# Kernel tuning notes

Measured on AMD Instinct MI355X. Metric: run time of the kernel, lower is better.

## Reference

```python
import jax, jax.numpy as jnp
import numpy as np

N = 80000
E = 1280000
C_IN, HID, C_OUT = 3, 64, 1
DEPTH = 3
KS = [40000, 20000, 10000]  # ceil(0.5 * n) per pooling level
EPS = 1e-5


def gcn_conv(x, W, src, dst, ew, n, fill=2.0):
    # PyG GCNConv with add_self_loops=True; improved => self-loop weight fill=2.0
    h = x @ W                                           # [n, F]
    deg = jax.ops.segment_sum(ew, dst, num_segments=n) + fill
    dinv = jax.lax.rsqrt(deg)
    norm = dinv[src] * ew * dinv[dst]                   # [E]
    agg = jax.ops.segment_sum(norm[:, None] * h[src], dst, num_segments=n)
    return agg + (fill * dinv * dinv)[:, None] * h      # self-loop term


def batchnorm(x, gamma, beta):
    # BatchNorm1d in training mode: biased batch stats over the node dim
    mu = jnp.mean(x, axis=0)
    var = jnp.var(x, axis=0)
    return gamma * (x - mu) * jax.lax.rsqrt(var + EPS) + beta


def gcn_block(x, src, dst, ew, n, W, gamma, beta, fill=2.0):
    return jax.nn.relu(batchnorm(gcn_conv(x, W, src, dst, ew, n, fill), gamma, beta))


def topk_pool(x, src, dst, ew, w, k):
    # TopKPooling with ReLU nonlinearity: score = relu(x.w / ||w||)
    n = x.shape[0]
    score = jax.nn.relu(x @ w / jnp.linalg.norm(w))
    sc, perm = jax.lax.top_k(score, k)
    xk = x[perm] * sc[:, None]
    # filter_adj with fixed edge count: invalid edges get weight 0 (no-op in GCN)
    mapping = jnp.full((n,), -1, dtype=src.dtype).at[perm].set(
        jnp.arange(k, dtype=src.dtype))
    ns, nd = mapping[src], mapping[dst]
    valid = (ns >= 0) & (nd >= 0)
    ns = jnp.where(valid, ns, 0)
    nd = jnp.where(valid, nd, 0)
    new_ew = jnp.where(valid, ew, jnp.zeros((), ew.dtype))
    return xk, ns, nd, new_ew, perm


def _forward(x, edge_index, Wd, gd, bd, pw, Wu, gu, bu, W_out):
    src, dst = edge_index[0], edge_index[1]
    ew = jnp.ones(src.shape, x.dtype)
    n = x.shape[0]
    x = gcn_block(x, src, dst, ew, n, Wd[0], gd[0], bd[0])
    xs, sds, ews, perms = [x], [(src, dst)], [ew], []
    for i in range(DEPTH):
        x, src, dst, ew, perm = topk_pool(x, src, dst, ew, pw[i], KS[i])
        x = gcn_block(x, src, dst, ew, KS[i], Wd[i + 1], gd[i + 1], bd[i + 1])
        if i < DEPTH - 1:
            xs.append(x); sds.append((src, dst)); ews.append(ew)
        perms.append(perm)
    for i in range(DEPTH):
        j = DEPTH - 1 - i
        res = xs[j]; src, dst = sds[j]; ew = ews[j]; perm = perms[j]
        up = jnp.zeros_like(res).at[perm].set(x)
        x = res + up
        if i < DEPTH - 1:
            x = gcn_block(x, src, dst, ew, res.shape[0], Wu[i], gu[i], bu[i])
        else:
            x = jax.nn.sigmoid(
                gcn_conv(x, W_out, src, dst, ew, res.shape[0], fill=1.0))
    return x


def setup_inputs() -> dict:
    key = jax.random.key(0)
    ks = jax.random.split(key, 16)
    nrm = lambda k, shape: jax.random.normal(k, shape, jnp.float32) * 0.1
    inp = {
        "x": jax.random.normal(ks[0], (N, C_IN), jnp.float32),
        "edge_index": jax.random.randint(ks[1], (2, E), 0, N, jnp.int32),
    }
    dims = [(C_IN, HID)] + [(HID, HID)] * DEPTH
    ki = 2
    for l, (a, b) in enumerate(dims):
        inp[f"W_d{l}"] = nrm(ks[ki], (a, b)); ki += 1
        inp[f"g_d{l}"] = jnp.ones((b,), jnp.float32)
        inp[f"b_d{l}"] = jnp.zeros((b,), jnp.float32)
    for l in range(DEPTH):
        inp[f"pw{l}"] = nrm(ks[ki], (HID,)); ki += 1
    for l in range(DEPTH - 1):
        inp[f"W_u{l}"] = nrm(ks[ki], (HID, HID)); ki += 1
        inp[f"g_u{l}"] = jnp.ones((HID,), jnp.float32)
        inp[f"b_u{l}"] = jnp.zeros((HID,), jnp.float32)
    inp["W_out"] = nrm(ks[ki], (HID, C_OUT))
    return inp


def reference(x, edge_index, W_d0, g_d0, b_d0, W_d1, g_d1, b_d1, W_d2, g_d2,
              b_d2, W_d3, g_d3, b_d3, pw0, pw1, pw2, W_u0, g_u0, b_u0,
              W_u1, g_u1, b_u1, W_out):
    Wd = [W_d0, W_d1, W_d2, W_d3]
    gd = [g_d0, g_d1, g_d2, g_d3]
    bd = [b_d0, b_d1, b_d2, b_d3]
    pw = [pw0, pw1, pw2]
    Wu = [W_u0, W_u1]
    gu = [g_u0, g_u1]
    bu = [b_u0, b_u1]
    return _forward(x, edge_index, Wd, gd, bd, pw, Wu, gu, bu, W_out)
```

## Files before the change

### kernel.cpp

```cpp
#include <hip/hip_runtime.h>
#include <cstdint>
#include <utility>

#define NN0 80000
#define NE 1280000
#define MMB_GRID 2048
#define EB 2048
#define ENB 625

static inline int cdiv(int a, int b){ return (a+b-1)/b; }

__global__ void k_conv64(const int* __restrict__ rp, const int* __restrict__ col,
                         const float* __restrict__ dinv, const float* __restrict__ x,
                         const float* __restrict__ W, float* __restrict__ out,
                         float* __restrict__ part, int n){
  __shared__ float yl[4][64];
  __shared__ float ls[64], lq[64];
  int lane = threadIdx.x & 63, w = threadIdx.x >> 6;
  if (threadIdx.x < 64){ ls[threadIdx.x] = 0.f; lq[threadIdx.x] = 0.f; }
  __syncthreads();
  float sa = 0.f, sq = 0.f;
  int wid = blockIdx.x*4 + w, nw = gridDim.x*4;
  for (int i = wid; i < n; i += nw){
    int beg = rp[i], end = rp[i+1];
    float di = dinv[i];
    float y = 0.f;
    int j = beg;
    for (; j + 4 <= end; j += 4){
      int s0 = col[j], s1 = col[j+1], s2 = col[j+2], s3 = col[j+3];
      float y0 = dinv[s0]*x[s0*64+lane];
      float y1 = dinv[s1]*x[s1*64+lane];
      float y2 = dinv[s2]*x[s2*64+lane];
      float y3 = dinv[s3]*x[s3*64+lane];
      y += (y0+y1) + (y2+y3);
    }
    for (; j < end; j++){ int s = col[j]; y += dinv[s]*x[s*64+lane]; }
    y = di*y + 2.f*di*di*x[i*64+lane];
    yl[w][lane] = y;
    float acc = 0.f;
    #pragma unroll
    for (int k2 = 0; k2 < 64; k2++)
      acc += yl[w][k2]*W[k2*64+lane];
    out[i*64+lane] = acc;
    sa += acc; sq += acc*acc;
  }
  atomicAdd(&ls[lane], sa); atomicAdd(&lq[lane], sq);
  __syncthreads();
  if (threadIdx.x < 128)
    part[blockIdx.x*128 + threadIdx.x] =
      (threadIdx.x < 64) ? ls[threadIdx.x] : lq[threadIdx.x-64];
}

__global__ void k_conv3(const int* __restrict__ rp, const int* __restrict__ col,
                        const float* __restrict__ dinv, const float* __restrict__ x,
                        const float* __restrict__ W, float* __restrict__ out,
                        float* __restrict__ part, int n){
  __shared__ float ls[64], lq[64];
  int lane = threadIdx.x & 63, w = threadIdx.x >> 6;
  if (threadIdx.x < 64){ ls[threadIdx.x] = 0.f; lq[threadIdx.x] = 0.f; }
  __syncthreads();
  float wf0 = W[lane], wf1 = W[64+lane], wf2 = W[128+lane];
  float sa = 0.f, sq = 0.f;
  int wid = blockIdx.x*4 + w, nw = gridDim.x*4;
  for (int i = wid; i < n; i += nw){
    int beg = rp[i], end = rp[i+1];
    float a0 = 0.f, a1 = 0.f, a2 = 0.f;
    for (int j = beg + lane; j < end; j += 64){
      int s2 = col[j];
      float ds = dinv[s2];
      a0 += ds*x[s2*3+0]; a1 += ds*x[s2*3+1]; a2 += ds*x[s2*3+2];
    }
    for (int o = 32; o > 0; o >>= 1){
      a0 += __shfl_xor(a0, o); a1 += __shfl_xor(a1, o); a2 += __shfl_xor(a2, o);
    }
    float di = dinv[i];
    float sl = 2.f*di*di;
    a0 = di*a0 + sl*x[i*3+0];
    a1 = di*a1 + sl*x[i*3+1];
    a2 = di*a2 + sl*x[i*3+2];
    float s = a0*wf0 + a1*wf1 + a2*wf2;
    out[i*64+lane] = s; sa += s; sq += s*s;
  }
  atomicAdd(&ls[lane], sa); atomicAdd(&lq[lane], sq);
  __syncthreads();
  if (threadIdx.x < 128)
    part[blockIdx.x*128 + threadIdx.x] =
      (threadIdx.x < 64) ? ls[threadIdx.x] : lq[threadIdx.x-64];
}

__global__ void k_stats_reduce(const float* __restrict__ part, float* __restrict__ stats){
  int c = blockIdx.x, lane = threadIdx.x;
  float s = 0.f;
  for (int b = lane; b < MMB_GRID; b += 64) s += part[b*128 + c];
  for (int o = 32; o > 0; o >>= 1) s += __shfl_xor(s, o);
  if (lane == 0) stats[c] = s;
}

__global__ void k_matvec(const float* __restrict__ x, const float* __restrict__ W,
                         float* __restrict__ h1, int n){
  int lane = threadIdx.x & 63, w = threadIdx.x >> 6;
  int wid = blockIdx.x*4 + w, nw = gridDim.x*4;
  float wv = W[lane];
  for (int i = wid; i < n; i += nw){
    float v = x[i*64+lane]*wv;
    for (int o = 32; o > 0; o >>= 1) v += __shfl_xor(v, o);
    if (lane == 0) h1[i] = v;
  }
}

__global__ void k_ehist6(const int* __restrict__ key, int* __restrict__ hist, int shift){
  __shared__ int lh[64];
  if (threadIdx.x < 64) lh[threadIdx.x] = 0;
  __syncthreads();
  int base = blockIdx.x*EB + threadIdx.x;
  #pragma unroll
  for (int u = 0; u < 8; u++)
    atomicAdd(&lh[(key[base + u*256] >> shift) & 63], 1);
  __syncthreads();
  if (threadIdx.x < 64) hist[threadIdx.x*ENB + blockIdx.x] = lh[threadIdx.x];
}

__global__ void k_escatter6(const int* __restrict__ keyin, const int* __restrict__ valin,
                            int* __restrict__ keyout, int* __restrict__ valout,
                            const int* __restrict__ hist, int shift){
  __shared__ int dbase[64], run[64], wcnt[4][64];
  int t = threadIdx.x, lane = t & 63, w = t >> 6;
  if (t < 64){ dbase[t] = hist[t*ENB + blockIdx.x]; run[t] = 0; }
  __syncthreads();
  for (int u = 0; u < 8; u++){
    if (t < 64){ wcnt[0][t]=0; wcnt[1][t]=0; wcnt[2][t]=0; wcnt[3][t]=0; }
    __syncthreads();
    int g = blockIdx.x*EB + u*256 + t;
    int kk = keyin[g], vv = valin[g];
    int d = (kk >> shift) & 63;
    unsigned long long m = ~0ull;
    #pragma unroll
    for (int b = 0; b < 6; b++){
      unsigned long long bal = __ballot((d >> b) & 1);
      m &= ((d >> b) & 1) ? bal : ~bal;
    }
    int rnk = __popcll(m & ((1ull << lane) - 1ull));
    if (rnk == 0) wcnt[w][d] = __popcll(m);
    __syncthreads();
    int off2 = run[d] + rnk;
    for (int w2 = 0; w2 < w; w2++) off2 += wcnt[w2][d];
    int pos = dbase[d] + off2;
    keyout[pos] = kk; valout[pos] = vv;
    __syncthreads();
    if (t < 64) run[t] += wcnt[0][t] + wcnt[1][t] + wcnt[2][t] + wcnt[3][t];
    __syncthreads();
  }
}

__global__ void k_rp_search(const int* __restrict__ skey, int* __restrict__ rp,
                            float* __restrict__ dinvA, float* __restrict__ dinvB, int n){
  int i = blockIdx.x*blockDim.x + threadIdx.x;
  if (i >= n) return;
  int lo = 0, hi = NE;
  while (lo < hi){ int mid = (lo+hi)>>1; if (skey[mid] < i) lo = mid+1; else hi = mid; }
  int a = lo;
  lo = a; hi = NE;
  while (lo < hi){ int mid = (lo+hi)>>1; if (skey[mid] < i+1) lo = mid+1; else hi = mid; }
  int b2 = lo;
  rp[i] = a;
  if (i == n-1) rp[n] = NE;
  float deg = (float)(b2 - a);
  dinvA[i] = 1.0f/sqrtf(deg + 2.f);
  dinvB[i] = 1.0f/sqrtf(deg + 1.f);
}

__global__ void k_scan_part(const int* __restrict__ in, int* __restrict__ bsum, int n){
  __shared__ int ws[256];
  int base = blockIdx.x*2048 + threadIdx.x*8;
  int s = 0;
  #pragma unroll
  for (int u = 0; u < 8; u++){ int i = base+u; if (i < n) s += in[i]; }
  ws[threadIdx.x] = s; __syncthreads();
  for (int st = 128; st > 0; st >>= 1){
    if (threadIdx.x < st) ws[threadIdx.x] += ws[threadIdx.x+st];
    __syncthreads();
  }
  if (threadIdx.x == 0) bsum[blockIdx.x] = ws[0];
}

__global__ void k_scan_fin_rp(const int* __restrict__ in, const int* __restrict__ bsum, int nb,
                              int* __restrict__ rp, float* __restrict__ dinvA, int n){
  __shared__ int bws[256]; __shared__ int ws[256];
  int t = threadIdx.x;
  bws[t] = (t < nb) ? bsum[t] : 0; __syncthreads();
  for (int st = 1; st < 256; st <<= 1){
    int a = (t >= st) ? bws[t-st] : 0; __syncthreads();
    bws[t] += a; __syncthreads();
  }
  int blockoff = (blockIdx.x == 0) ? 0 : bws[blockIdx.x-1];
  int base = blockIdx.x*2048 + t*8;
  int v[8]; int s = 0;
  #pragma unroll
  for (int u = 0; u < 8; u++){ int i = base+u; v[u] = (i < n) ? in[i] : 0; s += v[u]; }
  ws[t] = s; __syncthreads();
  for (int st = 1; st < 256; st <<= 1){
    int a = (t >= st) ? ws[t-st] : 0; __syncthreads();
    ws[t] += a; __syncthreads();
  }
  int off = blockoff + ws[t] - s;
  #pragma unroll
  for (int u = 0; u < 8; u++){
    int i = base+u;
    if (i < n){
      rp[i] = off; off += v[u];
      dinvA[i] = 1.0f/sqrtf((float)v[u] + 2.f);
      if (i == n-1) rp[n] = off;
    }
  }
}

__global__ void k_scan_fin_flat(int* __restrict__ data, const int* __restrict__ bsum, int nb, int n){
  __shared__ int bws[256]; __shared__ int ws[256];
  int t = threadIdx.x;
  bws[t] = (t < nb) ? bsum[t] : 0; __syncthreads();
  for (int st = 1; st < 256; st <<= 1){
    int a = (t >= st) ? bws[t-st] : 0; __syncthreads();
    bws[t] += a; __syncthreads();
  }
  int blockoff = (blockIdx.x == 0) ? 0 : bws[blockIdx.x-1];
  int base = blockIdx.x*2048 + t*8;
  int v[8]; int s = 0;
  #pragma unroll
  for (int u = 0; u < 8; u++){ int i = base+u; v[u] = (i < n) ? data[i] : 0; s += v[u]; }
  ws[t] = s; __syncthreads();
  for (int st = 1; st < 256; st <<= 1){
    int a = (t >= st) ? ws[t-st] : 0; __syncthreads();
    ws[t] += a; __syncthreads();
  }
  int off = blockoff + ws[t] - s;
  #pragma unroll
  for (int u = 0; u < 8; u++){
    int i = base+u;
    if (i < n){ data[i] = off; off += v[u]; }
  }
}

__global__ void k_hist_mapped(const int* __restrict__ rp_p, const int* __restrict__ col_p,
                              const int* __restrict__ mapv, int* __restrict__ indeg, int np){
  int d = blockIdx.x*blockDim.x + threadIdx.x;
  if (d >= np) return;
  int md = mapv[d];
  if (md < 0) return;
  int c = 0, e = rp_p[d+1];
  int j = rp_p[d];
  for (; j + 4 <= e; j += 4){
    int c0 = (mapv[col_p[j]]   >= 0);
    int c1 = (mapv[col_p[j+1]] >= 0);
    int c2 = (mapv[col_p[j+2]] >= 0);
    int c3 = (mapv[col_p[j+3]] >= 0);
    c += (c0+c1) + (c2+c3);
  }
  for (; j < e; j++) if (mapv[col_p[j]] >= 0) c++;
  indeg[md] = c;
}
__global__ void k_scatter_mapped(const int* __restrict__ rp_p, const int* __restrict__ col_p,
                                 const int* __restrict__ mapv, const int* __restrict__ rp_c,
                                 int* __restrict__ col_c, int np){
  int d = blockIdx.x*blockDim.x + threadIdx.x;
  if (d >= np) return;
  int md = mapv[d];
  if (md < 0) return;
  int pos = rp_c[md], e = rp_p[d+1];
  int j = rp_p[d];
  for (; j + 4 <= e; j += 4){
    int m0 = mapv[col_p[j]], m1 = mapv[col_p[j+1]];
    int m2 = mapv[col_p[j+2]], m3 = mapv[col_p[j+3]];
    if (m0 >= 0) col_c[pos++] = m0;
    if (m1 >= 0) col_c[pos++] = m1;
    if (m2 >= 0) col_c[pos++] = m2;
    if (m3 >= 0) col_c[pos++] = m3;
  }
  for (; j < e; j++){
    int ms = mapv[col_p[j]];
    if (ms >= 0) col_c[pos++] = ms;
  }
}

__global__ void k_gather_sig(const int* __restrict__ rp, const int* __restrict__ col,
                             const float* __restrict__ dinv, const float* __restrict__ h1,
                             float* __restrict__ out, int n){
  int i = blockIdx.x*blockDim.x + threadIdx.x;
  if (i >= n) return;
  int beg = rp[i], end = rp[i+1];
  float di = dinv[i];
  float acc = 0.f;
  int j = beg;
  for (; j + 4 <= end; j += 4){
    int s0 = col[j], s1 = col[j+1], s2 = col[j+2], s3 = col[j+3];
    float v0 = dinv[s0]*h1[s0];
    float v1 = dinv[s1]*h1[s1];
    float v2 = dinv[s2]*h1[s2];
    float v3 = dinv[s3]*h1[s3];
    acc += (v0+v1) + (v2+v3);
  }
  for (; j < end; j++) acc += dinv[col[j]]*h1[col[j]];
  float v = di*acc + di*di*h1[i];
  out[i] = 1.f/(1.f+expf(-v));
}

__global__ void k_bnrelu_scatter(const float* __restrict__ x, const float* __restrict__ stats,
                                 const float* __restrict__ gamma, const float* __restrict__ beta,
                                 const int* __restrict__ perm, float* __restrict__ res, int n){
  int t = blockIdx.x*blockDim.x + threadIdx.x;
  if (t >= n*64) return;
  int r = t >> 6, f = t & 63;
  float inv_n = 1.0f/(float)n;
  float mu = stats[f]*inv_n;
  float var = stats[64+f]*inv_n - mu*mu;
  float v = gamma[f]*(x[t]-mu)*(1.0f/sqrtf(var+1e-5f)) + beta[f];
  res[perm[r]*64+f] += fmaxf(v, 0.f);
}

__global__ void k_bnrelu_score(float* __restrict__ x, const float* __restrict__ stats,
                               const float* __restrict__ gamma, const float* __restrict__ beta,
                               const float* __restrict__ pw,
                               float* __restrict__ score, unsigned* __restrict__ key,
                               int* __restrict__ idx, int n, int P){
  int lane = threadIdx.x & 63, w = threadIdx.x >> 6;
  int wid = blockIdx.x*4 + w, nw = gridDim.x*4;
  float inv_n = 1.f/(float)n;
  float mu = stats[lane]*inv_n;
  float var = stats[64+lane]*inv_n - mu*mu;
  float gs = gamma[lane]*(1.f/sqrtf(var+1e-5f));
  float bt = beta[lane];
  float pv = pw[lane];
  float q = pv*pv;
  for (int o = 32; o > 0; o >>= 1) q += __shfl_xor(q, o);
  float qn = 1.f/sqrtf(q);
  for (int i = wid; i < n; i += nw){
    float v = fmaxf(gs*(x[i*64+lane]-mu)+bt, 0.f);
    x[i*64+lane] = v;
    float s = v*pv;
    for (int o = 32; o > 0; o >>= 1) s += __shfl_xor(s, o);
    if (lane == 0){
      float sc = fmaxf(s*qn, 0.f);
      score[i] = sc; key[i] = ~__float_as_uint(sc); idx[i] = i;
    }
  }
  for (int g = n + wid; g < P; g += nw)
    if (lane == 0){ key[g] = 0xFFFFFFFFu; idx[g] = 0; }
}

__global__ void k_radix_hist(const unsigned* __restrict__ key, int* __restrict__ hist,
                             int shift, int nblk){
  __shared__ int lh[256];
  lh[threadIdx.x] = 0; __syncthreads();
  int base = blockIdx.x*1024 + threadIdx.x;
  #pragma unroll
  for (int u = 0; u < 4; u++){
    unsigned d = (key[base + u*256] >> shift) & 255u;
    atomicAdd(&lh[d], 1);
  }
  __syncthreads();
  hist[threadIdx.x*nblk + blockIdx.x] = lh[threadIdx.x];
}

__global__ void k_radix_scatter(const unsigned* __restrict__ keyin, const int* __restrict__ idxin,
                                unsigned* __restrict__ keyout, int* __restrict__ idxout,
                                const int* __restrict__ hist, int shift, int nblk){
  __shared__ int dbase[256], run[256], sc[256];
  __shared__ int wcnt[4][256];
  int t = threadIdx.x, lane = t & 63, w = t >> 6;
  int pre = 0, tot = 0;
  for (int b = 0; b < nblk; b++){
    int v = hist[t*nblk + b];
    if (b < blockIdx.x) pre += v;
    tot += v;
  }
  sc[t] = tot; __syncthreads();
  for (int st = 1; st < 256; st <<= 1){
    int a = (t >= st) ? sc[t-st] : 0; __syncthreads();
    sc[t] += a; __syncthreads();
  }
  dbase[t] = sc[t] - tot + pre;
  run[t] = 0;
  for (int u = 0; u < 4; u++){
    wcnt[0][t] = 0; wcnt[1][t] = 0; wcnt[2][t] = 0; wcnt[3][t] = 0;
    __syncthreads();
    int g = blockIdx.x*1024 + u*256 + t;
    unsigned kk = keyin[g]; int id = idxin[g];
    unsigned d = (kk >> shift) & 255u;
    unsigned long long m = ~0ull;
    #pragma unroll
    for (int b = 0; b < 8; b++){
      unsigned long long bal = __ballot((d >> b) & 1u);
      m &= ((d >> b) & 1u) ? bal : ~bal;
    }
    int rnk = __popcll(m & ((1ull << lane) - 1ull));
    if (rnk == 0) wcnt[w][d] = __popcll(m);
    __syncthreads();
    int off2 = run[d] + rnk;
    for (int w2 = 0; w2 < w; w2++) off2 += wcnt[w2][d];
    int pos = dbase[d] + off2;
    keyout[pos] = kk; idxout[pos] = id;
    __syncthreads();
    run[t] += wcnt[0][t] + wcnt[1][t] + wcnt[2][t] + wcnt[3][t];
    __syncthreads();
  }
}

__global__ void k_select_gather(const int* __restrict__ idxs, const float* __restrict__ x,
                                const float* __restrict__ score, int* __restrict__ perm,
                                int* __restrict__ mapv, float* __restrict__ xk, int n, int k){
  int t = blockIdx.x*blockDim.x + threadIdx.x;
  if (t < n){
    int i = idxs[t];
    mapv[i] = (t < k) ? t : -1;
    if (t < k) perm[t] = i;
  }
  if (t < k*64){
    int r = t >> 6, f = t & 63;
    int i = idxs[r];
    xk[t] = x[i*64+f]*score[i];
  }
}

extern "C" void kernel_launch(void* const* d_in, const int* in_sizes, int n_in,
                              void* d_out, int out_size, void* d_ws, size_t ws_size,
                              hipStream_t stream) {
  const float* x_in = (const float*)d_in[0];
  const int* ei = (const int*)d_in[1];
  const int* src0 = ei;
  const int* dst0 = ei + NE;
  const float* W_d[4] = {(const float*)d_in[2],(const float*)d_in[5],(const float*)d_in[8],(const float*)d_in[11]};
  const float* g_d[4] = {(const float*)d_in[3],(const float*)d_in[6],(const float*)d_in[9],(const float*)d_in[12]};
  const float* b_d[4] = {(const float*)d_in[4],(const float*)d_in[7],(const float*)d_in[10],(const float*)d_in[13]};
  const float* pw[3]  = {(const float*)d_in[14],(const float*)d_in[15],(const float*)d_in[16]};
  const float* W_u[2] = {(const float*)d_in[17],(const float*)d_in[20]};
  const float* g_u[2] = {(const float*)d_in[18],(const float*)d_in[21]};
  const float* b_u[2] = {(const float*)d_in[19],(const float*)d_in[22]};
  const float* W_out  = (const float*)d_in[23];
  float* out = (float*)d_out;

  float* base = (float*)d_ws;
  size_t off = 0;
  auto alloc = [&](size_t nf){ float* p = base + off; off += nf; return p; };
  float* x0 = alloc(5120000);
  float* x1 = alloc(2560000);
  float* x2 = alloc(1280000);
  float* x3 = alloc(640000);
  float* A  = alloc(2560000);
  int* col0 = (int*)alloc(NE);
  int* col1 = (int*)alloc(NE);
  int* col2 = (int*)alloc(NE);
  int* col3 = (int*)alloc(NE);
  int* ek1 = (int*)alloc(NE);
  int* ev1 = (int*)alloc(NE);
  int* ek2 = (int*)alloc(NE);
  int* ev2 = (int*)alloc(NE);
  int* rp0 = (int*)alloc(80001);
  int* rp1 = (int*)alloc(40001);
  int* rp2 = (int*)alloc(20001);
  int* rp3 = (int*)alloc(10001);
  int* indeg  = (int*)alloc(NN0);
  float* dinv0  = alloc(NN0);
  float* dinv0f = alloc(NN0);
  float* dinv1  = alloc(40000);
  float* dinv2  = alloc(20000);
  float* dinv3  = alloc(10000);
  float* score = alloc(NN0);
  int* mapv = (int*)alloc(NN0);
  int* p0 = (int*)alloc(40000);
  int* p1 = (int*)alloc(20000);
  int* p2 = (int*)alloc(10000);
  float* stats = alloc(128);
  float* part  = alloc(MMB_GRID*128);
  unsigned* keyA = (unsigned*)alloc(81920);
  unsigned* keyB = (unsigned*)alloc(81920);
  int* idxA = (int*)alloc(81920);
  int* idxB = (int*)alloc(81920);
  int* hist = (int*)alloc(81920);
  int* ehist = (int*)alloc(64*ENB);
  int* bsum = (int*)alloc(256);
  (void)ws_size; (void)in_sizes; (void)n_in; (void)out_size;

  const int B = 256;

  auto scan_flat = [&](int* data, int n2){
    int nb = cdiv(n2, 2048);
    k_scan_part    <<<nb, 256, 0, stream>>>(data, bsum, n2);
    k_scan_fin_flat<<<nb, 256, 0, stream>>>(data, bsum, nb, n2);
  };
  auto scan_csr = [&](const int* indeg_, int* rp, float* dv, int n2){
    int nb = cdiv(n2, 2048);
    k_scan_part  <<<nb, 256, 0, stream>>>(indeg_, bsum, n2);
    k_scan_fin_rp<<<nb, 256, 0, stream>>>(indeg_, bsum, nb, rp, dv, n2);
  };

  auto conv = [&](const float* xin, const float* W, int n,
                  const int* rp, const int* col, const float* dv, float* dstb){
    k_conv64<<<MMB_GRID, B, 0, stream>>>(rp, col, dv, xin, W, dstb, part, n);
    k_stats_reduce<<<128, 64, 0, stream>>>(part, stats);
  };

  auto pool = [&](float* xb, const float* g, const float* bt, const float* w,
                  int n, int k, int* pm, float* xk){
    int nblk = cdiv(n, 1024), P = nblk*1024;
    k_bnrelu_score<<<1024, B, 0, stream>>>(xb, stats, g, bt, w, score, keyA, idxA, n, P);
    unsigned* ka = keyA; int* ia = idxA; unsigned* kb = keyB; int* ib = idxB;
    for (int pass = 0; pass < 4; pass++){
      k_radix_hist   <<<nblk, 256, 0, stream>>>(ka, hist, pass*8, nblk);
      k_radix_scatter<<<nblk, 256, 0, stream>>>(ka, ia, kb, ib, hist, pass*8, nblk);
      std::swap(ka, kb); std::swap(ia, ib);
    }
    k_select_gather<<<cdiv(k*64,B), B, 0, stream>>>(ia, xb, score, pm, mapv, xk, n, k);
  };

  auto csr_mapped = [&](const int* rp_p, const int* col_p, int np, int nc,
                        int* rp_c, int* col_c, float* dv){
    k_hist_mapped<<<cdiv(np,B), B, 0, stream>>>(rp_p, col_p, mapv, indeg, np);
    scan_csr(indeg, rp_c, dv, nc);
    k_scatter_mapped<<<cdiv(np,B), B, 0, stream>>>(rp_p, col_p, mapv, rp_c, col_c, np);
  };

  k_ehist6   <<<ENB, B, 0, stream>>>(dst0, ehist, 0);
  scan_flat(ehist, 64*ENB);
  k_escatter6<<<ENB, B, 0, stream>>>(dst0, src0, ek1, ev1, ehist, 0);
  k_ehist6   <<<ENB, B, 0, stream>>>(ek1, ehist, 6);
  scan_flat(ehist, 64*ENB);
  k_escatter6<<<ENB, B, 0, stream>>>(ek1, ev1, ek2, ev2, ehist, 6);
  k_ehist6   <<<ENB, B, 0, stream>>>(ek2, ehist, 12);
  scan_flat(ehist, 64*ENB);
  k_escatter6<<<ENB, B, 0, stream>>>(ek2, ev2, ek1, col0, ehist, 12);
  k_rp_search<<<cdiv(NN0,B), B, 0, stream>>>(ek1, rp0, dinv0, dinv0f, NN0);

  k_conv3<<<MMB_GRID, B, 0, stream>>>(rp0, col0, dinv0, x_in, W_d[0], x0, part, NN0);
  k_stats_reduce<<<128, 64, 0, stream>>>(part, stats);
  pool(x0, g_d[0], b_d[0], pw[0], NN0, 40000, p0, A);
  csr_mapped(rp0, col0, NN0, 40000, rp1, col1, dinv1);

  conv(A, W_d[1], 40000, rp1, col1, dinv1, x1);
  pool(x1, g_d[1], b_d[1], pw[1], 40000, 20000, p1, A);
  csr_mapped(rp1, col1, 40000, 20000, rp2, col2, dinv2);

  conv(A, W_d[2], 20000, rp2, col2, dinv2, x2);
  pool(x2, g_d[2], b_d[2], pw[2], 20000, 10000, p2, A);
  csr_mapped(rp2, col2, 20000, 10000, rp3, col3, dinv3);

  conv(A, W_d[3], 10000, rp3, col3, dinv3, x3);

  k_bnrelu_scatter<<<cdiv(10000*64,B), B, 0, stream>>>(x3, stats, g_d[3], b_d[3], p2, x2, 10000);
  conv(x2, W_u[0], 20000, rp2, col2, dinv2, A);
  k_bnrelu_scatter<<<cdiv(20000*64,B), B, 0, stream>>>(A, stats, g_u[0], b_u[0], p1, x1, 20000);
  conv(x1, W_u[1], 40000, rp1, col1, dinv1, A);
  k_bnrelu_scatter<<<cdiv(40000*64,B), B, 0, stream>>>(A, stats, g_u[1], b_u[1], p0, x0, 40000);

  float* h1 = score;
  k_matvec<<<512, B, 0, stream>>>(x0, W_out, h1, NN0);
  k_gather_sig<<<cdiv(NN0,B), B, 0, stream>>>(rp0, col0, dinv0f, h1, out, NN0);
}
```

Measured before the change: 740.8 us.

## Build initial CSR with one coarse bucket pass plus per-bucket LDS sort

Replaces the three-pass 6-bit radix sort of edges by destination with a single coarse pass keyed on bits 11+ of the destination, followed by a per-bucket kernel that counts, scans and scatters edges in shared memory to produce rp, col and both dinv arrays directly. This removes two histogram/scan/scatter rounds and the binary-search row-pointer kernel. The mapped-CSR scan is merged into one kernel that recomputes each block's prefix by summing all earlier inputs. Column order within a row becomes nondeterministic because of LDS atomics, which can change floating-point summation order.

```diff
diff --git a/kernel.cpp b/kernel.cpp
--- a/kernel.cpp
+++ b/kernel.cpp
@@ -1,6 +1,5 @@
 #include <hip/hip_runtime.h>
 #include <cstdint>
-#include <utility>
 
 #define NN0 80000
 #define NE 1280000
@@ -9,6 +8,179 @@
 #define ENB 625
 
 static inline int cdiv(int a, int b){ return (a+b-1)/b; }
+
+__global__ void k_ehist6(const int* __restrict__ key, int* __restrict__ hist, int shift){
+  __shared__ int lh[64];
+  if (threadIdx.x < 64) lh[threadIdx.x] = 0;
+  __syncthreads();
+  int base = blockIdx.x*EB + threadIdx.x;
+  #pragma unroll
+  for (int u = 0; u < 8; u++)
+    atomicAdd(&lh[(key[base + u*256] >> shift) & 63], 1);
+  __syncthreads();
+  if (threadIdx.x < 64) hist[threadIdx.x*ENB + blockIdx.x] = lh[threadIdx.x];
+}
+
+__global__ void k_scan_part(const int* __restrict__ in, int* __restrict__ bsum, int n){
+  __shared__ int ws[256];
+  int base = blockIdx.x*2048 + threadIdx.x*8;
+  int s = 0;
+  #pragma unroll
+  for (int u = 0; u < 8; u++){ int i = base+u; if (i < n) s += in[i]; }
+  ws[threadIdx.x] = s; __syncthreads();
+  for (int st = 128; st > 0; st >>= 1){
+    if (threadIdx.x < st) ws[threadIdx.x] += ws[threadIdx.x+st];
+    __syncthreads();
+  }
+  if (threadIdx.x == 0) bsum[blockIdx.x] = ws[0];
+}
+
+__global__ void k_scan_fin_flat(int* __restrict__ data, const int* __restrict__ bsum, int nb, int n){
+  __shared__ int bws[256]; __shared__ int ws[256];
+  int t = threadIdx.x;
+  bws[t] = (t < nb) ? bsum[t] : 0; __syncthreads();
+  for (int st = 1; st < 256; st <<= 1){
+    int a = (t >= st) ? bws[t-st] : 0; __syncthreads();
+    bws[t] += a; __syncthreads();
+  }
+  int blockoff = (blockIdx.x == 0) ? 0 : bws[blockIdx.x-1];
+  int base = blockIdx.x*2048 + t*8;
+  int v[8]; int s = 0;
+  #pragma unroll
+  for (int u = 0; u < 8; u++){ int i = base+u; v[u] = (i < n) ? data[i] : 0; s += v[u]; }
+  ws[t] = s; __syncthreads();
+  for (int st = 1; st < 256; st <<= 1){
+    int a = (t >= st) ? ws[t-st] : 0; __syncthreads();
+    ws[t] += a; __syncthreads();
+  }
+  int off = blockoff + ws[t] - s;
+  #pragma unroll
+  for (int u = 0; u < 8; u++){
+    int i = base+u;
+    if (i < n){ data[i] = off; off += v[u]; }
+  }
+}
+
+__global__ void k_escatter6(const int* __restrict__ keyin, const int* __restrict__ valin,
+                            int* __restrict__ keyout, int* __restrict__ valout,
+                            const int* __restrict__ hist, int shift){
+  __shared__ int dbase[64], run[64], wcnt[4][64];
+  int t = threadIdx.x, lane = t & 63, w = t >> 6;
+  if (t < 64){ dbase[t] = hist[t*ENB + blockIdx.x]; run[t] = 0; }
+  __syncthreads();
+  for (int u = 0; u < 8; u++){
+    if (t < 64){ wcnt[0][t]=0; wcnt[1][t]=0; wcnt[2][t]=0; wcnt[3][t]=0; }
+    __syncthreads();
+    int g = blockIdx.x*EB + u*256 + t;
+    int kk = keyin[g], vv = valin[g];
+    int d = (kk >> shift) & 63;
+    unsigned long long m = ~0ull;
+    #pragma unroll
+    for (int b = 0; b < 6; b++){
+      unsigned long long bal = __ballot((d >> b) & 1);
+      m &= ((d >> b) & 1) ? bal : ~bal;
+    }
+    int rnk = __popcll(m & ((1ull << lane) - 1ull));
+    if (rnk == 0) wcnt[w][d] = __popcll(m);
+    __syncthreads();
+    int off2 = run[d] + rnk;
+    for (int w2 = 0; w2 < w; w2++) off2 += wcnt[w2][d];
+    int pos = dbase[d] + off2;
+    keyout[pos] = kk; valout[pos] = vv;
+    __syncthreads();
+    if (t < 64) run[t] += wcnt[0][t] + wcnt[1][t] + wcnt[2][t] + wcnt[3][t];
+    __syncthreads();
+  }
+}
+
+__global__ __launch_bounds__(1024) void k_bucket_build(
+    const int* __restrict__ ek, const int* __restrict__ ev,
+    const int* __restrict__ hist_s,
+    int* __restrict__ rp, int* __restrict__ col,
+    float* __restrict__ dA, float* __restrict__ dB, int n){
+  __shared__ int cnt[2048];
+  __shared__ int sa[1024], sb[1024];
+  int b = blockIdx.x, t = threadIdx.x;
+  int gb = hist_s[b*ENB];
+  int ge = hist_s[(b+1)*ENB];
+  int n0 = b*2048;
+  cnt[t] = 0; cnt[t+1024] = 0;
+  __syncthreads();
+  for (int e = gb + t; e < ge; e += 1024)
+    atomicAdd(&cnt[ek[e] - n0], 1);
+  __syncthreads();
+  int v0 = cnt[2*t], v1 = cnt[2*t+1];
+  int s = v0 + v1;
+  sa[t] = s; __syncthreads();
+  int* cu = sa; int* ot = sb;
+  for (int st = 1; st < 1024; st <<= 1){
+    ot[t] = cu[t] + ((t >= st) ? cu[t-st] : 0);
+    __syncthreads();
+    int* tmp = cu; cu = ot; ot = tmp;
+  }
+  int base2 = cu[t] - s;
+  int p0 = base2, p1 = base2 + v0;
+  int nn = n - n0; if (nn > 2048) nn = 2048;
+  cnt[2*t]   = gb + p0;
+  cnt[2*t+1] = gb + p1;
+  int i0 = n0 + 2*t;
+  if (2*t < nn){
+    rp[i0] = gb + p0;
+    dA[i0] = 1.0f/sqrtf((float)v0 + 2.f);
+    dB[i0] = 1.0f/sqrtf((float)v0 + 1.f);
+  }
+  if (2*t+1 < nn){
+    rp[i0+1] = gb + p1;
+    dA[i0+1] = 1.0f/sqrtf((float)v1 + 2.f);
+    dB[i0+1] = 1.0f/sqrtf((float)v1 + 1.f);
+  }
+  if (b == (int)gridDim.x - 1 && t == 0) rp[n] = ge;
+  __syncthreads();
+  for (int e = gb + t; e < ge; e += 1024){
+    int d = ek[e];
+    int pos = atomicAdd(&cnt[d - n0], 1);
+    col[pos] = ev[e];
+  }
+}
+
+__global__ void k_scan_rp(const int* __restrict__ in, int* __restrict__ rp,
+                          int* __restrict__ cur, float* __restrict__ dA,
+                          float* __restrict__ dB, int n){
+  __shared__ int ws[256];
+  int t = threadIdx.x;
+  int pre = blockIdx.x*2048;
+  int s = 0;
+  for (int i = t; i < pre; i += 256) s += in[i];
+  ws[t] = s; __syncthreads();
+  for (int st = 128; st > 0; st >>= 1){
+    if (t < st) ws[t] += ws[t+st];
+    __syncthreads();
+  }
+  int blockoff = ws[0];
+  __syncthreads();
+  int base = pre + t*8;
+  int v[8]; int ls = 0;
+  #pragma unroll
+  for (int u = 0; u < 8; u++){ int i = base+u; v[u] = (i < n) ? in[i] : 0; ls += v[u]; }
+  ws[t] = ls; __syncthreads();
+  for (int st = 1; st < 256; st <<= 1){
+    int a = (t >= st) ? ws[t-st] : 0; __syncthreads();
+    ws[t] += a; __syncthreads();
+  }
+  int off = blockoff + ws[t] - ls;
+  #pragma unroll
+  for (int u = 0; u < 8; u++){
+    int i = base+u;
+    if (i < n){
+      rp[i] = off;
+      if (cur) cur[i] = off;
+      off += v[u];
+      dA[i] = 1.0f/sqrtf((float)v[u] + 2.f);
+      if (dB) dB[i] = 1.0f/sqrtf((float)v[u] + 1.f);
+      if (i == n-1) rp[n] = off;
+    }
+  }
+}
 
 __global__ void k_conv64(const int* __restrict__ rp, const int* __restrict__ col,
                          const float* __restrict__ dinv, const float* __restrict__ x,
@@ -94,226 +266,6 @@
   for (int b = lane; b < MMB_GRID; b += 64) s += part[b*128 + c];
   for (int o = 32; o > 0; o >>= 1) s += __shfl_xor(s, o);
   if (lane == 0) stats[c] = s;
-}
-
-__global__ void k_matvec(const float* __restrict__ x, const float* __restrict__ W,
-                         float* __restrict__ h1, int n){
-  int lane = threadIdx.x & 63, w = threadIdx.x >> 6;
-  int wid = blockIdx.x*4 + w, nw = gridDim.x*4;
-  float wv = W[lane];
-  for (int i = wid; i < n; i += nw){
-    float v = x[i*64+lane]*wv;
-    for (int o = 32; o > 0; o >>= 1) v += __shfl_xor(v, o);
-    if (lane == 0) h1[i] = v;
-  }
-}
-
-__global__ void k_ehist6(const int* __restrict__ key, int* __restrict__ hist, int shift){
-  __shared__ int lh[64];
-  if (threadIdx.x < 64) lh[threadIdx.x] = 0;
-  __syncthreads();
-  int base = blockIdx.x*EB + threadIdx.x;
-  #pragma unroll
-  for (int u = 0; u < 8; u++)
-    atomicAdd(&lh[(key[base + u*256] >> shift) & 63], 1);
-  __syncthreads();
-  if (threadIdx.x < 64) hist[threadIdx.x*ENB + blockIdx.x] = lh[threadIdx.x];
-}
-
-__global__ void k_escatter6(const int* __restrict__ keyin, const int* __restrict__ valin,
-                            int* __restrict__ keyout, int* __restrict__ valout,
-                            const int* __restrict__ hist, int shift){
-  __shared__ int dbase[64], run[64], wcnt[4][64];
-  int t = threadIdx.x, lane = t & 63, w = t >> 6;
-  if (t < 64){ dbase[t] = hist[t*ENB + blockIdx.x]; run[t] = 0; }
-  __syncthreads();
-  for (int u = 0; u < 8; u++){
-    if (t < 64){ wcnt[0][t]=0; wcnt[1][t]=0; wcnt[2][t]=0; wcnt[3][t]=0; }
-    __syncthreads();
-    int g = blockIdx.x*EB + u*256 + t;
-    int kk = keyin[g], vv = valin[g];
-    int d = (kk >> shift) & 63;
-    unsigned long long m = ~0ull;
-    #pragma unroll
-    for (int b = 0; b < 6; b++){
-      unsigned long long bal = __ballot((d >> b) & 1);
-      m &= ((d >> b) & 1) ? bal : ~bal;
-    }
-    int rnk = __popcll(m & ((1ull << lane) - 1ull));
-    if (rnk == 0) wcnt[w][d] = __popcll(m);
-    __syncthreads();
-    int off2 = run[d] + rnk;
-    for (int w2 = 0; w2 < w; w2++) off2 += wcnt[w2][d];
-    int pos = dbase[d] + off2;
-    keyout[pos] = kk; valout[pos] = vv;
-    __syncthreads();
-    if (t < 64) run[t] += wcnt[0][t] + wcnt[1][t] + wcnt[2][t] + wcnt[3][t];
-    __syncthreads();
-  }
-}
-
-__global__ void k_rp_search(const int* __restrict__ skey, int* __restrict__ rp,
-                            float* __restrict__ dinvA, float* __restrict__ dinvB, int n){
-  int i = blockIdx.x*blockDim.x + threadIdx.x;
-  if (i >= n) return;
-  int lo = 0, hi = NE;
-  while (lo < hi){ int mid = (lo+hi)>>1; if (skey[mid] < i) lo = mid+1; else hi = mid; }
-  int a = lo;
-  lo = a; hi = NE;
-  while (lo < hi){ int mid = (lo+hi)>>1; if (skey[mid] < i+1) lo = mid+1; else hi = mid; }
-  int b2 = lo;
-  rp[i] = a;
-  if (i == n-1) rp[n] = NE;
-  float deg = (float)(b2 - a);
-  dinvA[i] = 1.0f/sqrtf(deg + 2.f);
-  dinvB[i] = 1.0f/sqrtf(deg + 1.f);
-}
-
-__global__ void k_scan_part(const int* __restrict__ in, int* __restrict__ bsum, int n){
-  __shared__ int ws[256];
-  int base = blockIdx.x*2048 + threadIdx.x*8;
-  int s = 0;
-  #pragma unroll
-  for (int u = 0; u < 8; u++){ int i = base+u; if (i < n) s += in[i]; }
-  ws[threadIdx.x] = s; __syncthreads();
-  for (int st = 128; st > 0; st >>= 1){
-    if (threadIdx.x < st) ws[threadIdx.x] += ws[threadIdx.x+st];
-    __syncthreads();
-  }
-  if (threadIdx.x == 0) bsum[blockIdx.x] = ws[0];
-}
-
-__global__ void k_scan_fin_rp(const int* __restrict__ in, const int* __restrict__ bsum, int nb,
-                              int* __restrict__ rp, float* __restrict__ dinvA, int n){
-  __shared__ int bws[256]; __shared__ int ws[256];
-  int t = threadIdx.x;
-  bws[t] = (t < nb) ? bsum[t] : 0; __syncthreads();
-  for (int st = 1; st < 256; st <<= 1){
-    int a = (t >= st) ? bws[t-st] : 0; __syncthreads();
-    bws[t] += a; __syncthreads();
-  }
-  int blockoff = (blockIdx.x == 0) ? 0 : bws[blockIdx.x-1];
-  int base = blockIdx.x*2048 + t*8;
-  int v[8]; int s = 0;
-  #pragma unroll
-  for (int u = 0; u < 8; u++){ int i = base+u; v[u] = (i < n) ? in[i] : 0; s += v[u]; }
-  ws[t] = s; __syncthreads();
-  for (int st = 1; st < 256; st <<= 1){
-    int a = (t >= st) ? ws[t-st] : 0; __syncthreads();
-    ws[t] += a; __syncthreads();
-  }
-  int off = blockoff + ws[t] - s;
-  #pragma unroll
-  for (int u = 0; u < 8; u++){
-    int i = base+u;
-    if (i < n){
-      rp[i] = off; off += v[u];
-      dinvA[i] = 1.0f/sqrtf((float)v[u] + 2.f);
-      if (i == n-1) rp[n] = off;
-    }
-  }
-}
-
-__global__ void k_scan_fin_flat(int* __restrict__ data, const int* __restrict__ bsum, int nb, int n){
-  __shared__ int bws[256]; __shared__ int ws[256];
-  int t = threadIdx.x;
-  bws[t] = (t < nb) ? bsum[t] : 0; __syncthreads();
-  for (int st = 1; st < 256; st <<= 1){
-    int a = (t >= st) ? bws[t-st] : 0; __syncthreads();
-    bws[t] += a; __syncthreads();
-  }
-  int blockoff = (blockIdx.x == 0) ? 0 : bws[blockIdx.x-1];
-  int base = blockIdx.x*2048 + t*8;
-  int v[8]; int s = 0;
-  #pragma unroll
-  for (int u = 0; u < 8; u++){ int i = base+u; v[u] = (i < n) ? data[i] : 0; s += v[u]; }
-  ws[t] = s; __syncthreads();
-  for (int st = 1; st < 256; st <<= 1){
-    int a = (t >= st) ? ws[t-st] : 0; __syncthreads();
-    ws[t] += a; __syncthreads();
-  }
-  int off = blockoff + ws[t] - s;
-  #pragma unroll
-  for (int u = 0; u < 8; u++){
-    int i = base+u;
-    if (i < n){ data[i] = off; off += v[u]; }
-  }
-}
-
-__global__ void k_hist_mapped(const int* __restrict__ rp_p, const int* __restrict__ col_p,
-                              const int* __restrict__ mapv, int* __restrict__ indeg, int np){
-  int d = blockIdx.x*blockDim.x + threadIdx.x;
-  if (d >= np) return;
-  int md = mapv[d];
-  if (md < 0) return;
-  int c = 0, e = rp_p[d+1];
-  int j = rp_p[d];
-  for (; j + 4 <= e; j += 4){
-    int c0 = (mapv[col_p[j]]   >= 0);
-    int c1 = (mapv[col_p[j+1]] >= 0);
-    int c2 = (mapv[col_p[j+2]] >= 0);
-    int c3 = (mapv[col_p[j+3]] >= 0);
-    c += (c0+c1) + (c2+c3);
-  }
-  for (; j < e; j++) if (mapv[col_p[j]] >= 0) c++;
-  indeg[md] = c;
-}
-__global__ void k_scatter_mapped(const int* __restrict__ rp_p, const int* __restrict__ col_p,
-                                 const int* __restrict__ mapv, const int* __restrict__ rp_c,
-                                 int* __restrict__ col_c, int np){
-  int d = blockIdx.x*blockDim.x + threadIdx.x;
-  if (d >= np) return;
-  int md = mapv[d];
-  if (md < 0) return;
-  int pos = rp_c[md], e = rp_p[d+1];
-  int j = rp_p[d];
-  for (; j + 4 <= e; j += 4){
-    int m0 = mapv[col_p[j]], m1 = mapv[col_p[j+1]];
-    int m2 = mapv[col_p[j+2]], m3 = mapv[col_p[j+3]];
-    if (m0 >= 0) col_c[pos++] = m0;
-    if (m1 >= 0) col_c[pos++] = m1;
-    if (m2 >= 0) col_c[pos++] = m2;
-    if (m3 >= 0) col_c[pos++] = m3;
-  }
-  for (; j < e; j++){
-    int ms = mapv[col_p[j]];
-    if (ms >= 0) col_c[pos++] = ms;
-  }
-}
-
-__global__ void k_gather_sig(const int* __restrict__ rp, const int* __restrict__ col,
-                             const float* __restrict__ dinv, const float* __restrict__ h1,
-                             float* __restrict__ out, int n){
-  int i = blockIdx.x*blockDim.x + threadIdx.x;
-  if (i >= n) return;
-  int beg = rp[i], end = rp[i+1];
-  float di = dinv[i];
-  float acc = 0.f;
-  int j = beg;
-  for (; j + 4 <= end; j += 4){
-    int s0 = col[j], s1 = col[j+1], s2 = col[j+2], s3 = col[j+3];
-    float v0 = dinv[s0]*h1[s0];
-    float v1 = dinv[s1]*h1[s1];
-    float v2 = dinv[s2]*h1[s2];
-    float v3 = dinv[s3]*h1[s3];
-    acc += (v0+v1) + (v2+v3);
-  }
-  for (; j < end; j++) acc += dinv[col[j]]*h1[col[j]];
-  float v = di*acc + di*di*h1[i];
-  out[i] = 1.f/(1.f+expf(-v));
-}
-
-__global__ void k_bnrelu_scatter(const float* __restrict__ x, const float* __restrict__ stats,
-                                 const float* __restrict__ gamma, const float* __restrict__ beta,
-                                 const int* __restrict__ perm, float* __restrict__ res, int n){
-  int t = blockIdx.x*blockDim.x + threadIdx.x;
-  if (t >= n*64) return;
-  int r = t >> 6, f = t & 63;
-  float inv_n = 1.0f/(float)n;
-  float mu = stats[f]*inv_n;
-  float var = stats[64+f]*inv_n - mu*mu;
-  float v = gamma[f]*(x[t]-mu)*(1.0f/sqrtf(var+1e-5f)) + beta[f];
-  res[perm[r]*64+f] += fmaxf(v, 0.f);
 }
 
 __global__ void k_bnrelu_score(float* __restrict__ x, const float* __restrict__ stats,
@@ -420,6 +372,96 @@
   }
 }
 
+__global__ void k_hist_mapped(const int* __restrict__ rp_p, const int* __restrict__ col_p,
+                              const int* __restrict__ mapv, int* __restrict__ indeg, int np){
+  int d = blockIdx.x*blockDim.x + threadIdx.x;
+  if (d >= np) return;
+  int md = mapv[d];
+  if (md < 0) return;
+  int c = 0, e = rp_p[d+1];
+  int j = rp_p[d];
+  for (; j + 4 <= e; j += 4){
+    int c0 = (mapv[col_p[j]]   >= 0);
+    int c1 = (mapv[col_p[j+1]] >= 0);
+    int c2 = (mapv[col_p[j+2]] >= 0);
+    int c3 = (mapv[col_p[j+3]] >= 0);
+    c += (c0+c1) + (c2+c3);
+  }
+  for (; j < e; j++) if (mapv[col_p[j]] >= 0) c++;
+  indeg[md] = c;
+}
+
+__global__ void k_scatter_mapped(const int* __restrict__ rp_p, const int* __restrict__ col_p,
+                                 const int* __restrict__ mapv, const int* __restrict__ rp_c,
+                                 int* __restrict__ col_c, int np){
+  int d = blockIdx.x*blockDim.x + threadIdx.x;
+  if (d >= np) return;
+  int md = mapv[d];
+  if (md < 0) return;
+  int pos = rp_c[md], e = rp_p[d+1];
+  int j = rp_p[d];
+  for (; j + 4 <= e; j += 4){
+    int m0 = mapv[col_p[j]], m1 = mapv[col_p[j+1]];
+    int m2 = mapv[col_p[j+2]], m3 = mapv[col_p[j+3]];
+    if (m0 >= 0) col_c[pos++] = m0;
+    if (m1 >= 0) col_c[pos++] = m1;
+    if (m2 >= 0) col_c[pos++] = m2;
+    if (m3 >= 0) col_c[pos++] = m3;
+  }
+  for (; j < e; j++){
+    int ms = mapv[col_p[j]];
+    if (ms >= 0) col_c[pos++] = ms;
+  }
+}
+
+__global__ void k_bnrelu_scatter(const float* __restrict__ x, const float* __restrict__ stats,
+                                 const float* __restrict__ gamma, const float* __restrict__ beta,
+                                 const int* __restrict__ perm, float* __restrict__ res, int n){
+  int t = blockIdx.x*blockDim.x + threadIdx.x;
+  if (t >= n*64) return;
+  int r = t >> 6, f = t & 63;
+  float inv_n = 1.0f/(float)n;
+  float mu = stats[f]*inv_n;
+  float var = stats[64+f]*inv_n - mu*mu;
+  float v = gamma[f]*(x[t]-mu)*(1.0f/sqrtf(var+1e-5f)) + beta[f];
+  res[perm[r]*64+f] += fmaxf(v, 0.f);
+}
+
+__global__ void k_matvec(const float* __restrict__ x, const float* __restrict__ W,
+                         float* __restrict__ h1, int n){
+  int lane = threadIdx.x & 63, w = threadIdx.x >> 6;
+  int wid = blockIdx.x*4 + w, nw = gridDim.x*4;
+  float wv = W[lane];
+  for (int i = wid; i < n; i += nw){
+    float v = x[i*64+lane]*wv;
+    for (int o = 32; o > 0; o >>= 1) v += __shfl_xor(v, o);
+    if (lane == 0) h1[i] = v;
+  }
+}
+
+__global__ void k_gather_sig(const int* __restrict__ rp, const int* __restrict__ col,
+                             const float* __restrict__ dinv, const float* __restrict__ h1,
+                             float* __restrict__ out, int n){
+  int i = blockIdx.x*blockDim.x + threadIdx.x;
+  if (i >= n) return;
+  int beg = rp[i], end = rp[i+1];
+  float di = dinv[i];
+  float acc = 0.f;
+  int j = beg;
+  for (; j + 4 <= end; j += 4){
+    int s0 = col[j], s1 = col[j+1], s2 = col[j+2], s3 = col[j+3];
+    float v0 = dinv[s0]*h1[s0];
+    float v1 = dinv[s1]*h1[s1];
+    float v2 = dinv[s2]*h1[s2];
+    float v3 = dinv[s3]*h1[s3];
+    acc += (v0+v1) + (v2+v3);
+  }
+  for (; j < end; j++) acc += dinv[col[j]]*h1[col[j]];
+  float v = di*acc + di*di*h1[i];
+  out[i] = 1.f/(1.f+expf(-v));
+}
+
+
 extern "C" void kernel_launch(void* const* d_in, const int* in_sizes, int n_in,
                               void* d_out, int out_size, void* d_ws, size_t ws_size,
                               hipStream_t stream) {
@@ -451,8 +493,6 @@
   int* col3 = (int*)alloc(NE);
   int* ek1 = (int*)alloc(NE);
   int* ev1 = (int*)alloc(NE);
-  int* ek2 = (int*)alloc(NE);
-  int* ev2 = (int*)alloc(NE);
   int* rp0 = (int*)alloc(80001);
   int* rp1 = (int*)alloc(40001);
   int* rp2 = (int*)alloc(20001);
@@ -481,16 +521,15 @@
 
   const int B = 256;
 
-  auto scan_flat = [&](int* data, int n2){
-    int nb = cdiv(n2, 2048);
-    k_scan_part    <<<nb, 256, 0, stream>>>(data, bsum, n2);
-    k_scan_fin_flat<<<nb, 256, 0, stream>>>(data, bsum, nb, n2);
-  };
-  auto scan_csr = [&](const int* indeg_, int* rp, float* dv, int n2){
-    int nb = cdiv(n2, 2048);
-    k_scan_part  <<<nb, 256, 0, stream>>>(indeg_, bsum, n2);
-    k_scan_fin_rp<<<nb, 256, 0, stream>>>(indeg_, bsum, nb, rp, dv, n2);
-  };
+  k_ehist6<<<ENB, B, 0, stream>>>(dst0, ehist, 11);
+  {
+    int nb = cdiv(64*ENB, 2048);
+    k_scan_part    <<<nb, B, 0, stream>>>(ehist, bsum, 64*ENB);
+    k_scan_fin_flat<<<nb, B, 0, stream>>>(ehist, bsum, nb, 64*ENB);
+  }
+  k_escatter6<<<ENB, B, 0, stream>>>(dst0, src0, ek1, ev1, ehist, 11);
+  k_bucket_build<<<cdiv(NN0,2048), 1024, 0, stream>>>(ek1, ev1, ehist, rp0, col0,
+                                                      dinv0, dinv0f, NN0);
 
   auto conv = [&](const float* xin, const float* W, int n,
                   const int* rp, const int* col, const float* dv, float* dstb){
@@ -498,48 +537,38 @@
     k_stats_reduce<<<128, 64, 0, stream>>>(part, stats);
   };
 
-  auto pool = [&](float* xb, const float* g, const float* bt, const float* w,
-                  int n, int k, int* pm, float* xk){
+  auto pool = [&](float* xb, const float* gm, const float* bt, const float* pwv,
+                  int n, int k, int* pm){
     int nblk = cdiv(n, 1024), P = nblk*1024;
-    k_bnrelu_score<<<1024, B, 0, stream>>>(xb, stats, g, bt, w, score, keyA, idxA, n, P);
+    k_bnrelu_score<<<1024, B, 0, stream>>>(xb, stats, gm, bt, pwv, score, keyA, idxA, n, P);
     unsigned* ka = keyA; int* ia = idxA; unsigned* kb = keyB; int* ib = idxB;
     for (int pass = 0; pass < 4; pass++){
-      k_radix_hist   <<<nblk, 256, 0, stream>>>(ka, hist, pass*8, nblk);
-      k_radix_scatter<<<nblk, 256, 0, stream>>>(ka, ia, kb, ib, hist, pass*8, nblk);
-      std::swap(ka, kb); std::swap(ia, ib);
-    }
-    k_select_gather<<<cdiv(k*64,B), B, 0, stream>>>(ia, xb, score, pm, mapv, xk, n, k);
+      k_radix_hist   <<<nblk, B, 0, stream>>>(ka, hist, pass*8, nblk);
+      k_radix_scatter<<<nblk, B, 0, stream>>>(ka, ia, kb, ib, hist, pass*8, nblk);
+      unsigned* tk = ka; ka = kb; kb = tk;
+      int* ti = ia; ia = ib; ib = ti;
+    }
+    k_select_gather<<<cdiv(k*64,B), B, 0, stream>>>(ia, xb, score, pm, mapv, A, n, k);
   };
 
   auto csr_mapped = [&](const int* rp_p, const int* col_p, int np, int nc,
                         int* rp_c, int* col_c, float* dv){
     k_hist_mapped<<<cdiv(np,B), B, 0, stream>>>(rp_p, col_p, mapv, indeg, np);
-    scan_csr(indeg, rp_c, dv, nc);
+    k_scan_rp<<<cdiv(nc,2048), B, 0, stream>>>(indeg, rp_c, nullptr, dv, nullptr, nc);
     k_scatter_mapped<<<cdiv(np,B), B, 0, stream>>>(rp_p, col_p, mapv, rp_c, col_c, np);
   };
 
-  k_ehist6   <<<ENB, B, 0, stream>>>(dst0, ehist, 0);
-  scan_flat(ehist, 64*ENB);
-  k_escatter6<<<ENB, B, 0, stream>>>(dst0, src0, ek1, ev1, ehist, 0);
-  k_ehist6   <<<ENB, B, 0, stream>>>(ek1, ehist, 6);
-  scan_flat(ehist, 64*ENB);
-  k_escatter6<<<ENB, B, 0, stream>>>(ek1, ev1, ek2, ev2, ehist, 6);
-  k_ehist6   <<<ENB, B, 0, stream>>>(ek2, ehist, 12);
-  scan_flat(ehist, 64*ENB);
-  k_escatter6<<<ENB, B, 0, stream>>>(ek2, ev2, ek1, col0, ehist, 12);
-  k_rp_search<<<cdiv(NN0,B), B, 0, stream>>>(ek1, rp0, dinv0, dinv0f, NN0);
-
   k_conv3<<<MMB_GRID, B, 0, stream>>>(rp0, col0, dinv0, x_in, W_d[0], x0, part, NN0);
   k_stats_reduce<<<128, 64, 0, stream>>>(part, stats);
-  pool(x0, g_d[0], b_d[0], pw[0], NN0, 40000, p0, A);
+  pool(x0, g_d[0], b_d[0], pw[0], NN0, 40000, p0);
   csr_mapped(rp0, col0, NN0, 40000, rp1, col1, dinv1);
 
   conv(A, W_d[1], 40000, rp1, col1, dinv1, x1);
-  pool(x1, g_d[1], b_d[1], pw[1], 40000, 20000, p1, A);
+  pool(x1, g_d[1], b_d[1], pw[1], 40000, 20000, p1);
   csr_mapped(rp1, col1, 40000, 20000, rp2, col2, dinv2);
 
   conv(A, W_d[2], 20000, rp2, col2, dinv2, x2);
-  pool(x2, g_d[2], b_d[2], pw[2], 20000, 10000, p2, A);
+  pool(x2, g_d[2], b_d[2], pw[2], 20000, 10000, p2);
   csr_mapped(rp2, col2, 20000, 10000, rp3, col3, dinv3);
 
   conv(A, W_d[3], 10000, rp3, col3, dinv3, x3);
```

After: 743.2 us. No clear change (+0.3%).
